# Optimization experiments

Hardware: AMD Instinct MI355X
Metric: run time of the kernel (lower is better)

## Reference

```python
import jax, jax.numpy as jnp
import numpy as np

C_CURV = 1.0          # manifold curvature c
MIN_NORM = 1e-15      # hgcn min-norm clamp
ATANH_EPS = 1e-6      # artanh arg clamp (fp32-safe version of hgcn's 1e-15)

N_NODES, DIM, N_EDGES, N_CLASSES = 100000, 128, 1000000, 4


def setup_inputs() -> dict:
    key = jax.random.key(0)
    k1, k2, k3 = jax.random.split(key, 3)
    x = jax.random.normal(k1, (N_NODES, DIM), dtype=jnp.float32)
    idx = jax.random.randint(k2, (N_EDGES, 2), 0, N_NODES, dtype=jnp.int64)
    W = jax.random.normal(k3, (2 * DIM, N_CLASSES), dtype=jnp.float32) * 0.05
    b = jnp.zeros((N_CLASSES,), dtype=jnp.float32)
    return {"x": x, "idx": idx, "W": W, "b": b}


def _logmap0(x, c):
    # PoincareBall.logmap0: scale = artanh(sqrt(c)*||x||) / (sqrt(c)*||x||)
    sqrt_c = c ** 0.5
    norm = jnp.maximum(jnp.linalg.norm(x, axis=-1, keepdims=True), MIN_NORM)
    a = jnp.clip(sqrt_c * norm, -1.0 + ATANH_EPS, 1.0 - ATANH_EPS)
    return (jnp.arctanh(a) / (sqrt_c * norm)) * x


def reference(x, idx, W, b):
    # proj_tan0 is identity for the Poincare ball
    h = _logmap0(x, C_CURV)                                   # [N, D]
    edge_feat = jnp.concatenate([h[idx[:, 0]], h[idx[:, 1]]], axis=1)  # [E, 2D]
    # Linear with identity activation (dropout=0 at inference)
    return edge_feat @ W + b                                  # [E, n_classes]
```

## Files before the change

kernel.cpp:

```cpp
#include <hip/hip_runtime.h>
#include <hip/hip_bf16.h>


#define DIM 128

typedef float f32x4 __attribute__((ext_vector_type(4)));
typedef int   i32x2 __attribute__((ext_vector_type(2)));

__global__ __launch_bounds__(256) void node_proj_kernel(
    const float* __restrict__ x, const float* __restrict__ W,
    const float* __restrict__ b, float* __restrict__ y, int n_nodes)
{
    __shared__ float wp[1152];
    const int t = threadIdx.x;
    {
        const int r = t & 127, h = t >> 7;
        const f32x4 wv = ((const f32x4*)W)[t];
        *(f32x4*)(wp + r * 8 + (r >> 2) * 4 + h * 4) = wv;
    }
    __syncthreads();

    const int lane = t & 63;
    const int li   = lane & 3;
    const int gid  = lane >> 2;
    const int wid  = blockIdx.x * (blockDim.x >> 6) + (t >> 6);
    const int n0   = wid * 32 + gid * 2;
    if (n0 >= n_nodes) return;
    const bool has1 = (n0 + 1) < n_nodes;
    const int  n1   = has1 ? (n0 + 1) : n0;

    const f32x4* xp0 = (const f32x4*)(x + (size_t)n0 * DIM + li * 4);
    const f32x4* xp1 = (const f32x4*)(x + (size_t)n1 * DIM + li * 4);
    const float* wl  = wp + li * 36;

    f32x4 A[8], B[8];
#pragma unroll
    for (int j = 0; j < 8; ++j) A[j] = xp0[j * 4];
#pragma unroll
    for (int j = 0; j < 8; ++j) B[j] = xp1[j * 4];

    float acc0[9], acc1[9];
#pragma unroll
    for (int i = 0; i < 9; ++i) { acc0[i] = 0.f; acc1[i] = 0.f; }

#pragma unroll
    for (int j = 0; j < 8; ++j) {
#pragma unroll
        for (int k = 0; k < 4; ++k) {
            const f32x4 wa = *(const f32x4*)(wl + j * 144 + k * 8);
            const f32x4 wb = *(const f32x4*)(wl + j * 144 + k * 8 + 4);
            const float a = A[j][k], bb = B[j][k];
            acc0[0] += a * a;        acc1[0] += bb * bb;
            acc0[1] += a * wa[0];    acc1[1] += bb * wa[0];
            acc0[2] += a * wa[1];    acc1[2] += bb * wa[1];
            acc0[3] += a * wa[2];    acc1[3] += bb * wa[2];
            acc0[4] += a * wa[3];    acc1[4] += bb * wa[3];
            acc0[5] += a * wb[0];    acc1[5] += bb * wb[0];
            acc0[6] += a * wb[1];    acc1[6] += bb * wb[1];
            acc0[7] += a * wb[2];    acc1[7] += bb * wb[2];
            acc0[8] += a * wb[3];    acc1[8] += bb * wb[3];
        }
    }

#pragma unroll
    for (int i = 0; i < 9; ++i) {
        acc0[i] += __shfl_xor(acc0[i], 1, 64);
        acc0[i] += __shfl_xor(acc0[i], 2, 64);
        acc1[i] += __shfl_xor(acc1[i], 1, 64);
        acc1[i] += __shfl_xor(acc1[i], 2, 64);
    }

    const bool second = (li & 1);
    const bool nodeB  = (li >= 2);

    const float sq = nodeB ? acc1[0] : acc0[0];
    const float w0 = second ? (nodeB ? acc1[5] : acc0[5]) : (nodeB ? acc1[1] : acc0[1]);
    const float w1 = second ? (nodeB ? acc1[6] : acc0[6]) : (nodeB ? acc1[2] : acc0[2]);
    const float w2 = second ? (nodeB ? acc1[7] : acc0[7]) : (nodeB ? acc1[3] : acc0[3]);
    const float w3 = second ? (nodeB ? acc1[8] : acc0[8]) : (nodeB ? acc1[4] : acc0[4]);

    float norm = fmaxf(sqrtf(sq), 1e-15f);
    const float aa  = fminf(norm, 1.0f - 1e-6f);
    const float art = 0.5f * log1pf(2.0f * aa / (1.0f - aa));
    const float scale = art / norm;

    const f32x4 bv4 = *(const f32x4*)b;
    f32x4 o;
    o[0] = w0 * scale + (second ? 0.f : bv4[0]);
    o[1] = w1 * scale + (second ? 0.f : bv4[1]);
    o[2] = w2 * scale + (second ? 0.f : bv4[2]);
    o[3] = w3 * scale + (second ? 0.f : bv4[3]);

    if (!(nodeB && !has1))
        *(f32x4*)(y + (size_t)n0 * 8 + li * 4) = o;
}

__global__ __launch_bounds__(256) void edge_kernel(
    const int* __restrict__ idx, const float* __restrict__ y,
    float* __restrict__ out, int n_edges, int half)
{
    const int t = blockIdx.x * blockDim.x + threadIdx.x;
    if (t >= half) return;
    const int e0 = t;
    const int e1 = t + half;
    const bool has1 = e1 < n_edges;

    const i32x2 i0 = __builtin_nontemporal_load((const i32x2*)idx + e0);
    const i32x2 i1 = has1 ? __builtin_nontemporal_load((const i32x2*)idx + e1)
                          : i0;

    const f32x4 a0 = *(const f32x4*)(y + (size_t)i0[0] * 8);
    const f32x4 c0 = *(const f32x4*)(y + (size_t)i0[1] * 8 + 4);
    const f32x4 a1 = *(const f32x4*)(y + (size_t)i1[0] * 8);
    const f32x4 c1 = *(const f32x4*)(y + (size_t)i1[1] * 8 + 4);

    const f32x4 o0 = a0 + c0;
    __builtin_nontemporal_store(o0, (f32x4*)out + e0);
    if (has1) {
        const f32x4 o1 = a1 + c1;
        __builtin_nontemporal_store(o1, (f32x4*)out + e1);
    }
}

extern "C" void kernel_launch(void* const* d_in, const int* in_sizes, int n_in,
                              void* d_out, int out_size, void* d_ws, size_t ws_size,
                              hipStream_t stream) {
    const float* x   = (const float*)d_in[0];
    const int*   idx = (const int*)d_in[1];
    const float* W   = (const float*)d_in[2];
    const float* b   = (const float*)d_in[3];
    float* out = (float*)d_out;

    const int n_nodes = in_sizes[0] / DIM;
    const int n_edges = in_sizes[1] / 2;

    float* y = (float*)d_ws;

    const int blocks1 = (n_nodes + 127) / 128;
    node_proj_kernel<<<blocks1, 256, 0, stream>>>(x, W, b, y, n_nodes);

    const int half    = (n_edges + 1) / 2;
    const int blocks2 = (half + 255) / 256;
    edge_kernel<<<blocks2, 256, 0, stream>>>(idx, y, out, n_edges, half);
}
```

Baseline: 33.38 us.

## Fuse node projection and edge gather into one persistent kernel with grid barrier

Replaces the two launches with a single persistent kernel of 512 blocks. Each block first grid-strides over nodes to compute the projected per-node values, then waits on a global atomic-counter barrier, then grid-strides over edges. The counter is reset with a memset before each launch. The goal is to remove the second kernel launch and the gap between kernels. In exchange it adds a memset, a spin barrier that relies on all 512 blocks being resident at once, and fewer blocks in flight for the memory-bound gather phase.

```diff
diff --git a/kernel.cpp b/kernel.cpp
--- a/kernel.cpp
+++ b/kernel.cpp
@@ -3,9 +3,141 @@
 
 
 #define DIM 128
+#define NBLOCKS 512
 
 typedef float f32x4 __attribute__((ext_vector_type(4)));
 typedef int   i32x2 __attribute__((ext_vector_type(2)));
+
+__device__ __forceinline__ void node_phase(
+    const float* __restrict__ x, const float* __restrict__ b,
+    float* __restrict__ y, const float* wl, int li, int gid,
+    int wave, int total_waves, int n_nodes)
+{
+    for (int base = wave * 32; base < n_nodes; base += total_waves * 32) {
+        const int n0 = base + gid * 2;
+        if (n0 >= n_nodes) continue;
+        const bool has1 = (n0 + 1) < n_nodes;
+        const int  n1   = has1 ? (n0 + 1) : n0;
+
+        const f32x4* xp0 = (const f32x4*)(x + (size_t)n0 * DIM + li * 4);
+        const f32x4* xp1 = (const f32x4*)(x + (size_t)n1 * DIM + li * 4);
+
+        f32x4 A[8], B[8];
+#pragma unroll
+        for (int j = 0; j < 8; ++j) A[j] = xp0[j * 4];
+#pragma unroll
+        for (int j = 0; j < 8; ++j) B[j] = xp1[j * 4];
+
+        float acc0[9], acc1[9];
+#pragma unroll
+        for (int i = 0; i < 9; ++i) { acc0[i] = 0.f; acc1[i] = 0.f; }
+
+#pragma unroll
+        for (int j = 0; j < 8; ++j) {
+#pragma unroll
+            for (int k = 0; k < 4; ++k) {
+                const f32x4 wa = *(const f32x4*)(wl + j * 144 + k * 8);
+                const f32x4 wb = *(const f32x4*)(wl + j * 144 + k * 8 + 4);
+                const float a = A[j][k], bb = B[j][k];
+                acc0[0] += a * a;        acc1[0] += bb * bb;
+                acc0[1] += a * wa[0];    acc1[1] += bb * wa[0];
+                acc0[2] += a * wa[1];    acc1[2] += bb * wa[1];
+                acc0[3] += a * wa[2];    acc1[3] += bb * wa[2];
+                acc0[4] += a * wa[3];    acc1[4] += bb * wa[3];
+                acc0[5] += a * wb[0];    acc1[5] += bb * wb[0];
+                acc0[6] += a * wb[1];    acc1[6] += bb * wb[1];
+                acc0[7] += a * wb[2];    acc1[7] += bb * wb[2];
+                acc0[8] += a * wb[3];    acc1[8] += bb * wb[3];
+            }
+        }
+
+#pragma unroll
+        for (int i = 0; i < 9; ++i) {
+            acc0[i] += __shfl_xor(acc0[i], 1, 64);
+            acc0[i] += __shfl_xor(acc0[i], 2, 64);
+            acc1[i] += __shfl_xor(acc1[i], 1, 64);
+            acc1[i] += __shfl_xor(acc1[i], 2, 64);
+        }
+
+        const bool second = (li & 1);
+        const bool nodeB  = (li >= 2);
+
+        const float sq = nodeB ? acc1[0] : acc0[0];
+        const float w0 = second ? (nodeB ? acc1[5] : acc0[5]) : (nodeB ? acc1[1] : acc0[1]);
+        const float w1 = second ? (nodeB ? acc1[6] : acc0[6]) : (nodeB ? acc1[2] : acc0[2]);
+        const float w2 = second ? (nodeB ? acc1[7] : acc0[7]) : (nodeB ? acc1[3] : acc0[3]);
+        const float w3 = second ? (nodeB ? acc1[8] : acc0[8]) : (nodeB ? acc1[4] : acc0[4]);
+
+        float norm = fmaxf(sqrtf(sq), 1e-15f);
+        const float aa  = fminf(norm, 1.0f - 1e-6f);
+        const float art = 0.5f * log1pf(2.0f * aa / (1.0f - aa));
+        const float scale = art / norm;
+
+        const f32x4 bv4 = *(const f32x4*)b;
+        f32x4 o;
+        o[0] = w0 * scale + (second ? 0.f : bv4[0]);
+        o[1] = w1 * scale + (second ? 0.f : bv4[1]);
+        o[2] = w2 * scale + (second ? 0.f : bv4[2]);
+        o[3] = w3 * scale + (second ? 0.f : bv4[3]);
+
+        if (!(nodeB && !has1))
+            *(f32x4*)(y + (size_t)n0 * 8 + li * 4) = o;
+    }
+}
+
+__device__ __forceinline__ void load_w_lds(float* wp, const float* __restrict__ W, int t)
+{
+    const int r = t & 127, h = t >> 7;
+    const f32x4 wv = ((const f32x4*)W)[t];
+    *(f32x4*)(wp + r * 8 + (r >> 2) * 4 + h * 4) = wv;
+}
+
+__global__ __launch_bounds__(256, 4) void fused_kernel(
+    const float* __restrict__ x, const int* __restrict__ idx,
+    const float* __restrict__ W, const float* __restrict__ b,
+    float* __restrict__ y, float* __restrict__ out,
+    unsigned int* __restrict__ barrier_ctr,
+    int n_nodes, int n_edges)
+{
+    __shared__ float wp[1152];
+    const int t = threadIdx.x;
+    load_w_lds(wp, W, t);
+    __syncthreads();
+
+    const int lane = t & 63;
+    const int li   = lane & 3;
+    const int gid  = lane >> 2;
+    const int wave = blockIdx.x * (blockDim.x >> 6) + (t >> 6);
+    const int total_waves = gridDim.x * (blockDim.x >> 6);
+
+    node_phase(x, b, y, wp + li * 36, li, gid, wave, total_waves, n_nodes);
+
+    __syncthreads();
+    if (t == 0) {
+        __threadfence();
+        __hip_atomic_fetch_add(barrier_ctr, 1u, __ATOMIC_RELAXED,
+                               __HIP_MEMORY_SCOPE_AGENT);
+        unsigned int v; int spins = 0;
+        do {
+            v = __hip_atomic_load(barrier_ctr, __ATOMIC_RELAXED,
+                                  __HIP_MEMORY_SCOPE_AGENT);
+            if (v >= (unsigned int)gridDim.x) break;
+            __builtin_amdgcn_s_sleep(2);
+        } while (++spins < (1 << 20));
+        __threadfence();
+    }
+    __syncthreads();
+
+    const int nthreads = gridDim.x * blockDim.x;
+    const i32x2* idx2 = (const i32x2*)idx;
+    for (int e = blockIdx.x * blockDim.x + t; e < n_edges; e += nthreads) {
+        const i32x2 ii = __builtin_nontemporal_load(idx2 + e);
+        const f32x4 a0 = *(const f32x4*)(y + (size_t)ii[0] * 8);
+        const f32x4 c0 = *(const f32x4*)(y + (size_t)ii[1] * 8 + 4);
+        const f32x4 o0 = a0 + c0;
+        __builtin_nontemporal_store(o0, (f32x4*)out + e);
+    }
+}
 
 __global__ __launch_bounds__(256) void node_proj_kernel(
     const float* __restrict__ x, const float* __restrict__ W,
@@ -13,112 +145,29 @@
 {
     __shared__ float wp[1152];
     const int t = threadIdx.x;
-    {
-        const int r = t & 127, h = t >> 7;
-        const f32x4 wv = ((const f32x4*)W)[t];
-        *(f32x4*)(wp + r * 8 + (r >> 2) * 4 + h * 4) = wv;
-    }
+    load_w_lds(wp, W, t);
     __syncthreads();
 
     const int lane = t & 63;
     const int li   = lane & 3;
     const int gid  = lane >> 2;
-    const int wid  = blockIdx.x * (blockDim.x >> 6) + (t >> 6);
-    const int n0   = wid * 32 + gid * 2;
-    if (n0 >= n_nodes) return;
-    const bool has1 = (n0 + 1) < n_nodes;
-    const int  n1   = has1 ? (n0 + 1) : n0;
-
-    const f32x4* xp0 = (const f32x4*)(x + (size_t)n0 * DIM + li * 4);
-    const f32x4* xp1 = (const f32x4*)(x + (size_t)n1 * DIM + li * 4);
-    const float* wl  = wp + li * 36;
-
-    f32x4 A[8], B[8];
-#pragma unroll
-    for (int j = 0; j < 8; ++j) A[j] = xp0[j * 4];
-#pragma unroll
-    for (int j = 0; j < 8; ++j) B[j] = xp1[j * 4];
-
-    float acc0[9], acc1[9];
-#pragma unroll
-    for (int i = 0; i < 9; ++i) { acc0[i] = 0.f; acc1[i] = 0.f; }
-
-#pragma unroll
-    for (int j = 0; j < 8; ++j) {
-#pragma unroll
-        for (int k = 0; k < 4; ++k) {
-            const f32x4 wa = *(const f32x4*)(wl + j * 144 + k * 8);
-            const f32x4 wb = *(const f32x4*)(wl + j * 144 + k * 8 + 4);
-            const float a = A[j][k], bb = B[j][k];
-            acc0[0] += a * a;        acc1[0] += bb * bb;
-            acc0[1] += a * wa[0];    acc1[1] += bb * wa[0];
-            acc0[2] += a * wa[1];    acc1[2] += bb * wa[1];
-            acc0[3] += a * wa[2];    acc1[3] += bb * wa[2];
-            acc0[4] += a * wa[3];    acc1[4] += bb * wa[3];
-            acc0[5] += a * wb[0];    acc1[5] += bb * wb[0];
-            acc0[6] += a * wb[1];    acc1[6] += bb * wb[1];
-            acc0[7] += a * wb[2];    acc1[7] += bb * wb[2];
-            acc0[8] += a * wb[3];    acc1[8] += bb * wb[3];
-        }
-    }
-
-#pragma unroll
-    for (int i = 0; i < 9; ++i) {
-        acc0[i] += __shfl_xor(acc0[i], 1, 64);
-        acc0[i] += __shfl_xor(acc0[i], 2, 64);
-        acc1[i] += __shfl_xor(acc1[i], 1, 64);
-        acc1[i] += __shfl_xor(acc1[i], 2, 64);
-    }
-
-    const bool second = (li & 1);
-    const bool nodeB  = (li >= 2);
-
-    const float sq = nodeB ? acc1[0] : acc0[0];
-    const float w0 = second ? (nodeB ? acc1[5] : acc0[5]) : (nodeB ? acc1[1] : acc0[1]);
-    const float w1 = second ? (nodeB ? acc1[6] : acc0[6]) : (nodeB ? acc1[2] : acc0[2]);
-    const float w2 = second ? (nodeB ? acc1[7] : acc0[7]) : (nodeB ? acc1[3] : acc0[3]);
-    const float w3 = second ? (nodeB ? acc1[8] : acc0[8]) : (nodeB ? acc1[4] : acc0[4]);
-
-    float norm = fmaxf(sqrtf(sq), 1e-15f);
-    const float aa  = fminf(norm, 1.0f - 1e-6f);
-    const float art = 0.5f * log1pf(2.0f * aa / (1.0f - aa));
-    const float scale = art / norm;
-
-    const f32x4 bv4 = *(const f32x4*)b;
-    f32x4 o;
-    o[0] = w0 * scale + (second ? 0.f : bv4[0]);
-    o[1] = w1 * scale + (second ? 0.f : bv4[1]);
-    o[2] = w2 * scale + (second ? 0.f : bv4[2]);
-    o[3] = w3 * scale + (second ? 0.f : bv4[3]);
-
-    if (!(nodeB && !has1))
-        *(f32x4*)(y + (size_t)n0 * 8 + li * 4) = o;
+    const int wave = blockIdx.x * (blockDim.x >> 6) + (t >> 6);
+    const int total_waves = gridDim.x * (blockDim.x >> 6);
+    node_phase(x, b, y, wp + li * 36, li, gid, wave, total_waves, n_nodes);
 }
 
 __global__ __launch_bounds__(256) void edge_kernel(
     const int* __restrict__ idx, const float* __restrict__ y,
-    float* __restrict__ out, int n_edges, int half)
-{
-    const int t = blockIdx.x * blockDim.x + threadIdx.x;
-    if (t >= half) return;
-    const int e0 = t;
-    const int e1 = t + half;
-    const bool has1 = e1 < n_edges;
-
-    const i32x2 i0 = __builtin_nontemporal_load((const i32x2*)idx + e0);
-    const i32x2 i1 = has1 ? __builtin_nontemporal_load((const i32x2*)idx + e1)
-                          : i0;
-
-    const f32x4 a0 = *(const f32x4*)(y + (size_t)i0[0] * 8);
-    const f32x4 c0 = *(const f32x4*)(y + (size_t)i0[1] * 8 + 4);
-    const f32x4 a1 = *(const f32x4*)(y + (size_t)i1[0] * 8);
-    const f32x4 c1 = *(const f32x4*)(y + (size_t)i1[1] * 8 + 4);
-
-    const f32x4 o0 = a0 + c0;
-    __builtin_nontemporal_store(o0, (f32x4*)out + e0);
-    if (has1) {
-        const f32x4 o1 = a1 + c1;
-        __builtin_nontemporal_store(o1, (f32x4*)out + e1);
+    float* __restrict__ out, int n_edges)
+{
+    const int nthreads = gridDim.x * blockDim.x;
+    const i32x2* idx2 = (const i32x2*)idx;
+    for (int e = blockIdx.x * blockDim.x + threadIdx.x; e < n_edges; e += nthreads) {
+        const i32x2 ii = __builtin_nontemporal_load(idx2 + e);
+        const f32x4 a0 = *(const f32x4*)(y + (size_t)ii[0] * 8);
+        const f32x4 c0 = *(const f32x4*)(y + (size_t)ii[1] * 8 + 4);
+        const f32x4 o0 = a0 + c0;
+        __builtin_nontemporal_store(o0, (f32x4*)out + e);
     }
 }
 
@@ -135,11 +184,18 @@
     const int n_edges = in_sizes[1] / 2;
 
     float* y = (float*)d_ws;
-
-    const int blocks1 = (n_nodes + 127) / 128;
-    node_proj_kernel<<<blocks1, 256, 0, stream>>>(x, W, b, y, n_nodes);
-
-    const int half    = (n_edges + 1) / 2;
-    const int blocks2 = (half + 255) / 256;
-    edge_kernel<<<blocks2, 256, 0, stream>>>(idx, y, out, n_edges, half);
-}
+    const size_t y_bytes = (size_t)n_nodes * 8 * sizeof(float);
+
+    if (ws_size >= y_bytes + 1024) {
+        unsigned int* ctr =
+            (unsigned int*)((char*)d_ws + ((ws_size - 64) & ~(size_t)63));
+        (void)hipMemsetAsync(ctr, 0, sizeof(unsigned int), stream);
+        fused_kernel<<<NBLOCKS, 256, 0, stream>>>(x, idx, W, b, y, out, ctr,
+                                                  n_nodes, n_edges);
+    } else {
+        const int blocks1 = (n_nodes + 127) / 128;
+        node_proj_kernel<<<blocks1, 256, 0, stream>>>(x, W, b, y, n_nodes);
+        const int blocks2 = 2048;
+        edge_kernel<<<blocks2, 256, 0, stream>>>(idx, y, out, n_edges);
+    }
+}
```

New measurement: 82.47 us. 147% more time.
